# Kernel optimization log

Hardware: AMD Instinct MI355X
Metric: run time of the kernel (lower is better)

## Reference

```python
import jax, jax.numpy as jnp
import numpy as np

N_NODES = 40000
N_EDGES = 480000
MULT = 64
NUM_SPECIES = 5
N_BASIS = 8
MLP_HIDDEN = 64
AVG_NEIGH = 12.0

INV8 = float(1.0 / np.sqrt(8.0))
INV64 = float(1.0 / np.sqrt(64.0))
INV128 = float(1.0 / np.sqrt(128.0))


def _poly_envelope(x):
    # e3nn.poly_envelope(5, 2) == DimeNet-style cutoff with p=6:
    # f(0)=1, first 5 derivatives zero at 0, f and 2 derivatives zero at 1.
    u = 1.0 - 28.0 * x**6 + 48.0 * x**7 - 21.0 * x**8
    return jnp.where(x < 1.0, u, 0.0)


def setup_inputs() -> dict:
    key = jax.random.key(0)
    ks = jax.random.split(key, 15)
    vectors = jax.random.uniform(ks[0], (N_EDGES, 3), jnp.float32, -0.5, 0.5)
    node_scalars = jax.random.normal(ks[1], (N_NODES, MULT), jnp.float32)
    node_vectors = jax.random.normal(ks[2], (N_NODES, MULT, 3), jnp.float32)
    node_specie = jax.random.randint(ks[3], (N_NODES,), 0, NUM_SPECIES)
    senders = jax.random.randint(ks[4], (N_EDGES,), 0, N_NODES)
    receivers = jax.random.randint(ks[5], (N_EDGES,), 0, N_NODES)
    # learned params (e3nn Linear weights ~ N(0,1), fwd divides by sqrt(fan_in))
    W_up_s = jax.random.normal(ks[6], (MULT, MULT), jnp.float32)
    W_up_v = jax.random.normal(ks[7], (MULT, MULT), jnp.float32)
    W_skip_s = jax.random.normal(ks[8], (NUM_SPECIES, MULT, 2 * MULT), jnp.float32)
    W_skip_v = jax.random.normal(ks[9], (NUM_SPECIES, MULT, MULT), jnp.float32)
    W_mlp1 = jax.random.normal(ks[10], (N_BASIS, MLP_HIDDEN), jnp.float32)
    W_mlp2 = jax.random.normal(ks[11], (MLP_HIDDEN, MLP_HIDDEN), jnp.float32)
    W_mlp3 = jax.random.normal(ks[12], (MLP_HIDDEN, 4 * MULT), jnp.float32)
    W_down_s = jax.random.normal(ks[13], (2 * MULT, 2 * MULT), jnp.float32)
    W_down_v = jax.random.normal(ks[14], (2 * MULT, MULT), jnp.float32)
    return dict(vectors=vectors, node_scalars=node_scalars, node_vectors=node_vectors,
                node_specie=node_specie, senders=senders, receivers=receivers,
                W_up_s=W_up_s, W_up_v=W_up_v, W_skip_s=W_skip_s, W_skip_v=W_skip_v,
                W_mlp1=W_mlp1, W_mlp2=W_mlp2, W_mlp3=W_mlp3,
                W_down_s=W_down_s, W_down_v=W_down_v)


def reference(vectors, node_scalars, node_vectors, node_specie, senders, receivers,
              W_up_s, W_up_v, W_skip_s, W_skip_v, W_mlp1, W_mlp2, W_mlp3,
              W_down_s, W_down_v):
    N = node_scalars.shape[0]
    # self-connection: species-indexed linear ('skip_tp'), output 128x0e + 64x1o
    sc_s = jnp.einsum('ni,nio->no', node_scalars, W_skip_s[node_specie]) * INV64
    sc_v = jnp.einsum('nic,nio->noc', node_vectors, W_skip_v[node_specie]) * INV64
    # linear_up (irreps-wise linear, 64x0e+64x1o -> same)
    h_s = (node_scalars @ W_up_s) * INV64
    h_v = jnp.einsum('nic,io->noc', node_vectors, W_up_v) * INV64
    # gather by sender
    m_s = h_s[senders]                       # [E,64]
    m_v = h_v[senders]                       # [E,64,3]
    # spherical harmonics l=1, normalize=True, component norm: sqrt(3)*r_hat
    lengths = jnp.linalg.norm(vectors, axis=1, keepdims=True)   # [E,1]
    safe_len = jnp.where(lengths == 0.0, 1.0, lengths)
    Y = jnp.sqrt(3.0) * vectors / safe_len                      # [E,3]
    # sparse CG tensor product (component norm): 0e x 1o -> 1o, 1o x 1o -> 0e
    tp_1o = m_s[:, :, None] * Y[:, None, :]                     # [E,64,3]
    tp_0e = jnp.einsum('eic,ec->ei', m_v, Y) / jnp.sqrt(3.0)    # [E,64]
    # concatenate + regroup -> 128x0e + 128x1o
    msg_s = jnp.concatenate([m_s, tp_0e], axis=1)               # [E,128]
    msg_v = jnp.concatenate([m_v, tp_1o], axis=1)               # [E,128,3]
    # radial basis (bessel, x_max=1) * smooth envelope
    k = jnp.arange(1, N_BASIS + 1, dtype=jnp.float32)
    bes = jnp.sqrt(2.0) * jnp.sin(k * jnp.pi * safe_len) / safe_len  # [E,8]
    rb = jnp.where(lengths == 0.0, 0.0, bes * _poly_envelope(lengths))
    h = jax.nn.swish((rb @ W_mlp1) * INV8)
    h = jax.nn.swish((h @ W_mlp2) * INV64)
    mix = (h @ W_mlp3) * INV64                                  # [E,256]
    msg_s = msg_s * mix[:, :128]
    msg_v = msg_v * mix[:, 128:, None]
    # scatter-add to receivers, normalize by sqrt(avg_num_neighbors)
    inv_sqrt_nn = 1.0 / np.sqrt(AVG_NEIGH)
    agg_s = jax.ops.segment_sum(msg_s, receivers, num_segments=N) * inv_sqrt_nn
    agg_v = jax.ops.segment_sum(msg_v, receivers, num_segments=N) * inv_sqrt_nn
    # linear_down to 128x0e + 64x1o, plus self-connection
    d_s = (agg_s @ W_down_s) * INV128 + sc_s                    # [N,128]
    d_v = jnp.einsum('nic,io->noc', agg_v, W_down_v) * INV128 + sc_v  # [N,64,3]
    # gate: first 64 scalars kept (swish), last 64 gate the vectors (swish)
    out_s = jax.nn.swish(d_s[:, :MULT])
    gates = jax.nn.swish(d_s[:, MULT:])
    out_v = d_v * gates[:, :, None]
    return jnp.concatenate([out_s, out_v.reshape(N, MULT * 3)], axis=1)  # [N,256]
```

## Files before the change

kernel.cpp:

```cpp
#include <hip/hip_runtime.h>
#include <hip/hip_bf16.h>

#define N_NODES 40000
#define N_EDGES 480000
#define SEG 2
#define SEG_E (N_EDGES / SEG)
#define SEG_TILES (SEG_E / 16)
#define SCAN_BLOCKS 157
#define TPW 2

typedef short bf16x8 __attribute__((ext_vector_type(8)));
typedef float f32x4 __attribute__((ext_vector_type(4)));

__device__ __forceinline__ float bf2f(__hip_bfloat16 x) { return __bfloat162float(x); }

__device__ __forceinline__ float swishf(float x) { return x / (1.0f + __expf(-x)); }

__device__ __forceinline__ float bflo(unsigned u) { union { unsigned u; float f; } w; w.u = u << 16; return w.f; }
__device__ __forceinline__ float bfhi(unsigned u) { union { unsigned u; float f; } w; w.u = u & 0xffff0000u; return w.f; }
__device__ __forceinline__ float bfu(unsigned short u) { union { unsigned u; float f; } w; w.u = ((unsigned)u) << 16; return w.f; }

__device__ __forceinline__ unsigned short f2bf_bits(float x) {
    union { __hip_bfloat16 h; unsigned short u; } c; c.h = __float2bfloat16(x); return c.u;
}

__constant__ const float INV8 = 0.35355339059327373f;
__constant__ const float INV64 = 0.125f;
__constant__ const float INV128 = 0.08838834764831845f;
__constant__ const float INV_NN = 0.2886751345948129f;
__constant__ const float SQRT2 = 1.4142135623730951f;
__constant__ const float SQRT3 = 1.7320508075688772f;
__constant__ const float INV_SQRT3 = 0.5773502691896258f;
__constant__ const float PI_F = 3.14159265358979323846f;

__device__ __forceinline__ float LDf(const void* p, size_t i, bool f32) {
    float v;
    if (f32) v = ((const float*)p)[i];
    else     v = bf2f(((const __hip_bfloat16*)p)[i]);
    return v;
}
__device__ __forceinline__ void load_f8r(const void* p, size_t i, bool f32, float* out) {
    if (f32) {
        const float4* q4 = (const float4*)((const float*)p + i);
        float4 a = q4[0], b = q4[1];
        out[0] = a.x; out[1] = a.y; out[2] = a.z; out[3] = a.w;
        out[4] = b.x; out[5] = b.y; out[6] = b.z; out[7] = b.w;
    } else {
        bf16x8 v = *(const bf16x8*)((const unsigned short*)p + i);
        #pragma unroll
        for (int j = 0; j < 8; j++) out[j] = bfu((unsigned short)v[j]);
    }
}

__global__ void detect_kernel(const unsigned short* __restrict__ w, int* __restrict__ flag) {
    int lane = threadIdx.x;
    int cnt = 0;
    for (int i = lane; i < 2048; i += 64) {
        unsigned e = (w[2 * i] >> 7) & 0xFF;
        if (e >= 110 && e <= 133) cnt++;
    }
    #pragma unroll
    for (int off = 32; off > 0; off >>= 1) cnt += __shfl_down(cnt, off, 64);
    if (lane == 0) *flag = (cnt > 1024) ? 1 : 0;
}

__global__ __launch_bounds__(256) void wprep_kernel(
    const void* __restrict__ W_up_s, const void* __restrict__ W_up_v,
    const void* __restrict__ W_skip_s, const void* __restrict__ W_skip_v,
    const void* __restrict__ W_down_s, const void* __restrict__ W_down_v,
    const void* __restrict__ W_mlp2, const void* __restrict__ W_mlp3,
    unsigned short* __restrict__ Wup_sq, unsigned short* __restrict__ Wup_vq,
    unsigned short* __restrict__ Wq_s, unsigned short* __restrict__ Wq_v,
    unsigned short* __restrict__ W2q, unsigned short* __restrict__ W3q,
    const int* __restrict__ flag)
{
    bool f32 = (*flag == 0);
    const float SC = INV128 * INV_NN;
    int gid = blockIdx.x * 256 + threadIdx.x;
    int gs = gridDim.x * 256;
    for (int i = gid; i < 4096; i += gs) {
        int o = i & 63, k = i >> 6;
        Wup_sq[o * 72 + k] = f2bf_bits(LDf(W_up_s, k * 64 + o, f32) * INV64);
        Wup_vq[o * 72 + k] = f2bf_bits(LDf(W_up_v, k * 64 + o, f32) * INV64);
    }
    for (int i = gid; i < 5 * 128 * 192; i += gs) {
        int sp = i / 24576, r = i - sp * 24576;
        int o = r / 192, k = r - o * 192;
        float w = (k < 128) ? LDf(W_down_s, k * 128 + o, f32) * SC
                            : LDf(W_skip_s, sp * 8192 + (k - 128) * 128 + o, f32) * INV64;
        Wq_s[sp * 25600 + o * 200 + k] = f2bf_bits(w);
    }
    for (int i = gid; i < 5 * 64 * 192; i += gs) {
        int sp = i / 12288, r = i - sp * 12288;
        int o = r / 192, k = r - o * 192;
        float w = (k < 128) ? LDf(W_down_v, k * 64 + o, f32) * SC
                            : LDf(W_skip_v, sp * 4096 + (k - 128) * 64 + o, f32) * INV64;
        Wq_v[sp * 12800 + o * 200 + k] = f2bf_bits(w);
    }
    for (int i = gid; i < 16384; i += gs) {
        int o = i & 255, k = i >> 8;
        W3q[o * 72 + k] = f2bf_bits(LDf(W_mlp3, k * 256 + o, f32));
    }
    for (int i = gid; i < 4096; i += gs) {
        int o = i & 63, k = i >> 6;
        W2q[o * 72 + k] = f2bf_bits(LDf(W_mlp2, k * 64 + o, f32));
    }
}

__global__ __launch_bounds__(256) void hist_kernel(const int* __restrict__ receivers,
                                                   int* __restrict__ cnt) {
    int e = blockIdx.x * 256 + threadIdx.x;
    if (e < N_EDGES) atomicAdd(&cnt[receivers[e]], 1);
}

__global__ __launch_bounds__(256) void partial_kernel(const int* __restrict__ cnt,
                                                      int* __restrict__ partials) {
    __shared__ int red[4];
    int idx = blockIdx.x * 256 + threadIdx.x;
    int v = (idx < N_NODES) ? cnt[idx] : 0;
    #pragma unroll
    for (int off = 32; off > 0; off >>= 1) v += __shfl_down(v, off, 64);
    int wave = threadIdx.x >> 6, lane = threadIdx.x & 63;
    if (lane == 0) red[wave] = v;
    __syncthreads();
    if (threadIdx.x == 0) partials[blockIdx.x] = red[0] + red[1] + red[2] + red[3];
}

__global__ __launch_bounds__(256) void scanp_kernel(const int* __restrict__ partials,
                                                    int* __restrict__ pscan) {
    __shared__ int buf[256];
    int t = threadIdx.x;
    int v = (t < SCAN_BLOCKS) ? partials[t] : 0;
    buf[t] = v;
    __syncthreads();
    for (int off = 1; off < 256; off <<= 1) {
        int tmp = (t >= off) ? buf[t - off] : 0;
        __syncthreads();
        buf[t] += tmp;
        __syncthreads();
    }
    if (t < SCAN_BLOCKS) pscan[t] = buf[t] - v;
}

__global__ __launch_bounds__(256) void offs_kernel(const int* __restrict__ cnt,
                                                   const int* __restrict__ pscan,
                                                   int* __restrict__ offs,
                                                   int* __restrict__ cursor) {
    __shared__ int buf[256];
    int b = blockIdx.x, t = threadIdx.x;
    int idx = b * 256 + t;
    int v = (idx < N_NODES) ? cnt[idx] : 0;
    buf[t] = v;
    __syncthreads();
    for (int off = 1; off < 256; off <<= 1) {
        int tmp = (t >= off) ? buf[t - off] : 0;
        __syncthreads();
        buf[t] += tmp;
        __syncthreads();
    }
    int exc = buf[t] - v + pscan[b];
    if (idx < N_NODES) { offs[idx] = exc; cursor[idx] = exc; }
    if (idx == N_NODES - 1) offs[N_NODES] = exc + v;
}

__global__ __launch_bounds__(256) void scatter_kernel(const int* __restrict__ receivers,
                                                      const int* __restrict__ senders,
                                                      const void* __restrict__ vectors,
                                                      int* __restrict__ cursor,
                                                      int* __restrict__ sorted_snd,
                                                      float4* __restrict__ sorted_vec,
                                                      const int* __restrict__ flag) {
    bool f32 = (*flag == 0);
    int e = blockIdx.x * 256 + threadIdx.x;
    if (e < N_EDGES) {
        float vx = LDf(vectors, (size_t)e * 3 + 0, f32);
        float vy = LDf(vectors, (size_t)e * 3 + 1, f32);
        float vz = LDf(vectors, (size_t)e * 3 + 2, f32);
        int p = atomicAdd(&cursor[receivers[e]], 1);
        sorted_snd[p] = senders[e];
        sorted_vec[p] = float4{vx, vy, vz, 0.f};
    }
}

__global__ __launch_bounds__(256) void hist5_kernel(const int* __restrict__ specie,
                                                    int* __restrict__ cnt5) {
    int n = blockIdx.x * 256 + threadIdx.x;
    int lane = threadIdx.x & 63;
    int sp = (n < N_NODES) ? specie[n] : -1;
    #pragma unroll
    for (int s = 0; s < 5; s++) {
        unsigned long long mask = __ballot(sp == s);
        if (mask != 0ull) {
            int leader = __builtin_ctzll(mask);
            if (lane == leader) atomicAdd(&cnt5[s], __popcll(mask));
        }
    }
}

__global__ void scan5_kernel(const int* __restrict__ cnt5, int* __restrict__ sp_offs,
                             int* __restrict__ cursor5, int* __restrict__ tile_info) {
    if (threadIdx.x != 0 || blockIdx.x != 0) return;
    int run = 0, tb = 0;
    for (int s = 0; s < 5; s++) {
        sp_offs[s] = run; cursor5[s] = run;
        tile_info[s] = tb;
        int c = cnt5[s];
        int T = (c + 15) >> 4;
        tile_info[8 + s] = T;
        tb += (T + 3) >> 2;
        run += c;
    }
    sp_offs[5] = run;
    tile_info[5] = tb;
}

__global__ __launch_bounds__(256) void scatter5_kernel(const int* __restrict__ specie,
                                                       int* __restrict__ cursor5,
                                                       int* __restrict__ sorted_node) {
    int n = blockIdx.x * 256 + threadIdx.x;
    int lane = threadIdx.x & 63;
    int sp = (n < N_NODES) ? specie[n] : -1;
    #pragma unroll
    for (int s = 0; s < 5; s++) {
        unsigned long long mask = __ballot(sp == s);
        if (mask != 0ull) {
            int leader = __builtin_ctzll(mask);
            int base = 0;
            if (lane == leader) base = atomicAdd(&cursor5[s], __popcll(mask));
            base = __shfl(base, leader);
            if (sp == s) {
                int prefix = __popcll(mask & ((1ull << lane) - 1ull));
                sorted_node[base + prefix] = n;
            }
        }
    }
}

__global__ __launch_bounds__(256) void node_up_kernel(
    const void* __restrict__ node_scalars,
    const void* __restrict__ node_vectors,
    const unsigned short* __restrict__ Wup_sq,
    const unsigned short* __restrict__ Wup_vq,
    unsigned short* __restrict__ hbuf,
    unsigned short* __restrict__ ns_b,
    unsigned short* __restrict__ nv_t,
    const int* __restrict__ flag)
{
    bool f32 = (*flag == 0);
    __shared__ __align__(16) unsigned short WsT[64 * 72];
    __shared__ __align__(16) unsigned short WvT[64 * 72];
    int tid = threadIdx.x;
    for (int i = tid; i < 576; i += 256) {
        ((uint4*)WsT)[i] = ((const uint4*)Wup_sq)[i];
        ((uint4*)WvT)[i] = ((const uint4*)Wup_vq)[i];
    }
    __syncthreads();
    int wave = tid >> 6, lane = tid & 63;
    int m = lane & 15, q = lane >> 4;
    int base = (blockIdx.x * 4 + wave) * 16;

    f32x4 accS[4];
    f32x4 accV[3][4];
    #pragma unroll
    for (int t = 0; t < 4; t++) {
        accS[t] = f32x4{0.f, 0.f, 0.f, 0.f};
        #pragma unroll
        for (int c = 0; c < 3; c++) accV[c][t] = f32x4{0.f, 0.f, 0.f, 0.f};
    }

    #pragma unroll
    for (int kk = 0; kk < 2; kk++) {
        int i0 = kk * 32 + 8 * q;
        float fs[8];
        load_f8r(node_scalars, (size_t)(base + m) * 64 + i0, f32, fs);
        bf16x8 aS;
        #pragma unroll
        for (int j = 0; j < 8; j++) aS[j] = (short)f2bf_bits(fs[j]);
        *(bf16x8*)(ns_b + (size_t)(base + m) * 64 + i0) = aS;
        float fv[24];
        size_t vbase = (size_t)(base + m) * 192 + (size_t)i0 * 3;
        load_f8r(node_vectors, vbase,      f32, fv);
        load_f8r(node_vectors, vbase + 8,  f32, fv + 8);
        load_f8r(node_vectors, vbase + 16, f32, fv + 16);
        bf16x8 aV[3];
        #pragma unroll
        for (int c = 0; c < 3; c++) {
            #pragma unroll
            for (int j = 0; j < 8; j++) aV[c][j] = (short)f2bf_bits(fv[3 * j + c]);
            *(bf16x8*)(nv_t + (size_t)c * N_NODES * 64 + (size_t)(base + m) * 64 + i0) = aV[c];
        }
        #pragma unroll
        for (int t = 0; t < 4; t++) {
            bf16x8 bS = *(const bf16x8*)(WsT + (16 * t + m) * 72 + kk * 32 + 8 * q);
            bf16x8 bV = *(const bf16x8*)(WvT + (16 * t + m) * 72 + kk * 32 + 8 * q);
            accS[t]    = __builtin_amdgcn_mfma_f32_16x16x32_bf16(aS,    bS, accS[t],    0, 0, 0);
            accV[0][t] = __builtin_amdgcn_mfma_f32_16x16x32_bf16(aV[0], bV, accV[0][t], 0, 0, 0);
            accV[1][t] = __builtin_amdgcn_mfma_f32_16x16x32_bf16(aV[1], bV, accV[1][t], 0, 0, 0);
            accV[2][t] = __builtin_amdgcn_mfma_f32_16x16x32_bf16(aV[2], bV, accV[2][t], 0, 0, 0);
        }
    }
    #pragma unroll
    for (int t = 0; t < 4; t++) {
        #pragma unroll
        for (int r = 0; r < 4; r++) {
            uint2 pk;
            pk.x = (unsigned)f2bf_bits(accS[t][r])    | ((unsigned)f2bf_bits(accV[0][t][r]) << 16);
            pk.y = (unsigned)f2bf_bits(accV[1][t][r]) | ((unsigned)f2bf_bits(accV[2][t][r]) << 16);
            *(uint2*)(hbuf + (size_t)(base + 4 * q + r) * 256 + (16 * t + m) * 4) = pk;
        }
    }
}

__global__ __launch_bounds__(512) void mlp_kernel(
    const float4* __restrict__ sorted_vec,
    const void* __restrict__ W1,
    const unsigned short* __restrict__ W2q,
    const unsigned short* __restrict__ W3q,
    unsigned short* __restrict__ mixseg,
    unsigned short* __restrict__ yq,
    int p_lo,
    const int* __restrict__ flag)
{
    bool f32 = (*flag == 0);
    __shared__ __align__(16) unsigned short W3T[256 * 72];
    __shared__ __align__(16) unsigned short W2T[64 * 72];
    __shared__ unsigned short hbl[8 * 64 * 18];
    int tid = threadIdx.x;
    for (int i = tid; i < 2304; i += 512) ((uint4*)W3T)[i] = ((const uint4*)W3q)[i];
    for (int i = tid; i < 576; i += 512)  ((uint4*)W2T)[i] = ((const uint4*)W2q)[i];
    __syncthreads();
    int wave = tid >> 6, lane = tid & 63;
    int m = lane & 15, q = lane >> 4;
    unsigned short* hb = hbl + wave * (64 * 18);
    f32x4 zero4 = {0.f, 0.f, 0.f, 0.f};

    bf16x8 a1f[4];
    #pragma unroll
    for (int t = 0; t < 4; t++) {
        #pragma unroll
        for (int j = 0; j < 8; j++) a1f[t][j] = 0;
        if (q == 0) {
            #pragma unroll
            for (int j = 0; j < 8; j++)
                a1f[t][j] = (short)f2bf_bits(LDf(W1, j * 64 + 16 * t + m, f32));
        }
    }

    int tile0 = (blockIdx.x * 8 + wave) * TPW;
    #pragma unroll 1
    for (int tt = 0; tt < TPW; tt++) {
        int tile = tile0 + tt;
        if (tile >= SEG_TILES) break;
        int p = p_lo + tile * 16 + m;

        float4 sv = sorted_vec[p];
        float vx = sv.x, vy = sv.y, vz = sv.z;
        float len2 = vx * vx + vy * vy + vz * vz;
        float len = sqrtf(len2);
        float Yx = 0.f, Yy = 0.f, Yz = 0.f;
        float rb[8];
        if (len > 0.f) {
            float inv = 1.f / len;
            Yx = SQRT3 * vx * inv; Yy = SQRT3 * vy * inv; Yz = SQRT3 * vz * inv;
            float x6 = len2 * len2 * len2;
            float env = (len < 1.f) ? fmaf(x6, fmaf(len, fmaf(len, -21.f, 48.f), -28.f), 1.f) : 0.f;
            float c = SQRT2 * inv * env;
            #pragma unroll
            for (int k = 0; k < 8; k++) rb[k] = c * __sinf((float)(k + 1) * PI_F * len);
        } else {
            #pragma unroll
            for (int k = 0; k < 8; k++) rb[k] = 0.f;
        }
        if (q == 0) {
            uint2 yw;
            yw.x = f2bf_bits(Yx) | ((unsigned)f2bf_bits(Yy) << 16);
            yw.y = f2bf_bits(Yz);
            *(uint2*)(yq + (size_t)p * 4) = yw;
        }

        bf16x8 b_rb;
        #pragma unroll
        for (int j = 0; j < 8; j++) b_rb[j] = (q == 0) ? (short)f2bf_bits(rb[j]) : (short)0;
        #pragma unroll
        for (int t = 0; t < 4; t++) {
            f32x4 c = __builtin_amdgcn_mfma_f32_16x16x32_bf16(a1f[t], b_rb, zero4, 0, 0, 0);
            #pragma unroll
            for (int r = 0; r < 4; r++)
                hb[(16 * t + 4 * q + r) * 18 + m] = f2bf_bits(swishf(c[r] * INV8));
        }
        bf16x8 b2[2];
        #pragma unroll
        for (int h = 0; h < 2; h++)
            #pragma unroll
            for (int j = 0; j < 8; j++)
                b2[h][j] = (short)hb[(32 * h + 8 * q + j) * 18 + m];
        #pragma unroll
        for (int t = 0; t < 4; t++) {
            bf16x8 a0 = *(const bf16x8*)(W2T + (16 * t + m) * 72 + 8 * q);
            bf16x8 a1 = *(const bf16x8*)(W2T + (16 * t + m) * 72 + 32 + 8 * q);
            f32x4 c = __builtin_amdgcn_mfma_f32_16x16x32_bf16(a0, b2[0], zero4, 0, 0, 0);
            c = __builtin_amdgcn_mfma_f32_16x16x32_bf16(a1, b2[1], c, 0, 0, 0);
            #pragma unroll
            for (int r = 0; r < 4; r++)
                hb[(16 * t + 4 * q + r) * 18 + m] = f2bf_bits(swishf(c[r] * INV64));
        }
        bf16x8 b3[2];
        #pragma unroll
        for (int h = 0; h < 2; h++)
            #pragma unroll
            for (int j = 0; j < 8; j++)
                b3[h][j] = (short)hb[(32 * h + 8 * q + j) * 18 + m];
        size_t rowbase = ((size_t)(tile * 16 + m)) * 256;
        #pragma unroll
        for (int t3 = 0; t3 < 16; t3++) {
            bf16x8 a0 = *(const bf16x8*)(W3T + (16 * t3 + m) * 72 + 8 * q);
            bf16x8 a1 = *(const bf16x8*)(W3T + (16 * t3 + m) * 72 + 32 + 8 * q);
            f32x4 c = __builtin_amdgcn_mfma_f32_16x16x32_bf16(a0, b3[0], zero4, 0, 0, 0);
            c = __builtin_amdgcn_mfma_f32_16x16x32_bf16(a1, b3[1], c, 0, 0, 0);
            uint2 v;
            v.x = f2bf_bits(c[0] * INV64) | ((unsigned)f2bf_bits(c[1] * INV64) << 16);
            v.y = f2bf_bits(c[2] * INV64) | ((unsigned)f2bf_bits(c[3] * INV64) << 16);
            *(uint2*)(mixseg + rowbase + 16 * t3 + 4 * q) = v;
        }
    }
}

__global__ __launch_bounds__(256) void agg_kernel(
    const unsigned short* __restrict__ hbuf,
    const int* __restrict__ sorted_snd,
    const unsigned short* __restrict__ mixseg,
    const unsigned short* __restrict__ yq,
    const int* __restrict__ offs,
    unsigned short* __restrict__ agg_s_b,
    unsigned short* __restrict__ agg_v_b,
    int slo, int shi)
{
    int tid = threadIdx.x, wave = tid >> 6, lane = tid & 63;
    int n = blockIdx.x * 4 + wave;
    if (n >= N_NODES) return;
    int beg = __builtin_amdgcn_readfirstlane(offs[n]);
    int end = __builtin_amdgcn_readfirstlane(offs[n + 1]);
    int lo = beg > slo ? beg : slo;
    int hi = end < shi ? end : shi;
    bool owner = (beg >= slo && beg < shi) || (beg >= shi && shi == N_EDGES);
    if (!owner && hi <= lo) return;
    unsigned short* aS = agg_s_b + (size_t)n * 128;
    unsigned short* aV = agg_v_b + (size_t)n * 384;
    float s0, s1, v0, v1, v2, v3, v4, v5;
    if (owner) {
        s0 = s1 = v0 = v1 = v2 = v3 = v4 = v5 = 0.f;
    } else {
        s0 = bfu(aS[lane]); s1 = bfu(aS[64 + lane]);
        v0 = bfu(aV[lane]); v1 = bfu(aV[64 + lane]); v2 = bfu(aV[128 + lane]);
        v3 = bfu(aV[192 + lane]); v4 = bfu(aV[256 + lane]); v5 = bfu(aV[320 + lane]);
    }
    for (int chunk = lo; chunk < hi; chunk += 64) {
        int cc = hi - chunk; if (cc > 64) cc = 64;
        int sv = (lane < cc) ? sorted_snd[chunk + lane] : 0;
        int i = 0;
        for (; i + 3 < cc; i += 4) {
            uint2 h[4]; uint2 yw[4];
            float mx[4][4];
            #pragma unroll
            for (int u = 0; u < 4; u++) {
                int snd = __builtin_amdgcn_readlane(sv, i + u);
                int p = chunk + i + u;
                h[u] = *(const uint2*)(hbuf + (size_t)snd * 256 + lane * 4);
                const unsigned short* mp = mixseg + (size_t)(p - slo) * 256;
                mx[u][0] = bfu(mp[lane]);       mx[u][1] = bfu(mp[64 + lane]);
                mx[u][2] = bfu(mp[128 + lane]); mx[u][3] = bfu(mp[192 + lane]);
                yw[u] = *(const uint2*)(yq + (size_t)p * 4);
            }
            #pragma unroll
            for (int u = 0; u < 4; u++) {
                float m_s = bflo(h[u].x), mv0 = bfhi(h[u].x), mv1 = bflo(h[u].y), mv2 = bfhi(h[u].y);
                float Yx = bflo(yw[u].x), Yy = bfhi(yw[u].x), Yz = bflo(yw[u].y);
                float tp0 = (mv0 * Yx + mv1 * Yy + mv2 * Yz) * INV_SQRT3;
                s0 = fmaf(m_s, mx[u][0], s0);
                s1 = fmaf(tp0, mx[u][1], s1);
                float t1 = m_s * mx[u][3];
                v0 = fmaf(mv0, mx[u][2], v0); v1 = fmaf(t1, Yx, v1);
                v2 = fmaf(mv1, mx[u][2], v2); v3 = fmaf(t1, Yy, v3);
                v4 = fmaf(mv2, mx[u][2], v4); v5 = fmaf(t1, Yz, v5);
            }
        }
        for (; i < cc; i++) {
            int snd = __builtin_amdgcn_readlane(sv, i);
            int p = chunk + i;
            uint2 hbv = *(const uint2*)(hbuf + (size_t)snd * 256 + lane * 4);
            const unsigned short* mp = mixseg + (size_t)(p - slo) * 256;
            float mix0 = bfu(mp[lane]), mix1 = bfu(mp[64 + lane]);
            float mix2 = bfu(mp[128 + lane]), mix3 = bfu(mp[192 + lane]);
            uint2 yw = *(const uint2*)(yq + (size_t)p * 4);
            float m_s = bflo(hbv.x), mv0 = bfhi(hbv.x), mv1 = bflo(hbv.y), mv2 = bfhi(hbv.y);
            float Yx = bflo(yw.x), Yy = bfhi(yw.x), Yz = bflo(yw.y);
            float tp0 = (mv0 * Yx + mv1 * Yy + mv2 * Yz) * INV_SQRT3;
            s0 = fmaf(m_s, mix0, s0);
            s1 = fmaf(tp0, mix1, s1);
            float t1 = m_s * mix3;
            v0 = fmaf(mv0, mix2, v0); v1 = fmaf(t1, Yx, v1);
            v2 = fmaf(mv1, mix2, v2); v3 = fmaf(t1, Yy, v3);
            v4 = fmaf(mv2, mix2, v4); v5 = fmaf(t1, Yz, v5);
        }
    }
    aS[lane] = f2bf_bits(s0); aS[64 + lane] = f2bf_bits(s1);
    aV[lane] = f2bf_bits(v0); aV[64 + lane] = f2bf_bits(v1); aV[128 + lane] = f2bf_bits(v2);
    aV[192 + lane] = f2bf_bits(v3); aV[256 + lane] = f2bf_bits(v4); aV[320 + lane] = f2bf_bits(v5);
}

__global__ __launch_bounds__(256) void node_final_kernel(
    const unsigned short* __restrict__ Wq_s,
    const unsigned short* __restrict__ Wq_v,
    const unsigned short* __restrict__ ns_b,
    const unsigned short* __restrict__ nv_t,
    const unsigned short* __restrict__ agg_s_b,
    const unsigned short* __restrict__ agg_v_b,
    const int* __restrict__ sorted_node,
    const int* __restrict__ sp_offs,
    const int* __restrict__ tile_info,
    void* __restrict__ out,
    const int* __restrict__ flag)
{
    bool f32 = (*flag == 0);
    int b = blockIdx.x;
    if (b >= tile_info[5]) return;
    __shared__ __align__(16) unsigned short As[128 * 200];
    __shared__ __align__(16) unsigned short Av[64 * 200];
    int sp = 0;
    #pragma unroll
    for (int s = 1; s < 5; s++) if (b >= tile_info[s]) sp = s;
    int tid = threadIdx.x;
    const uint4* ps = (const uint4*)(Wq_s + (size_t)sp * 25600);
    for (int i = tid; i < 3200; i += 256) ((uint4*)As)[i] = ps[i];
    const uint4* pv = (const uint4*)(Wq_v + (size_t)sp * 12800);
    for (int i = tid; i < 1600; i += 256) ((uint4*)Av)[i] = pv[i];
    __syncthreads();
    int wave = tid >> 6, lane = tid & 63;
    int m = lane & 15, q = lane >> 4;
    int T = tile_info[8 + sp];
    int tl = (b - tile_info[sp]) * 4 + wave;
    if (tl >= T) return;
    int row = sp_offs[sp] + tl * 16;
    int cnt = sp_offs[sp + 1] - row; if (cnt > 16) cnt = 16;
    int mm = (m < cnt) ? m : 0;
    int node = sorted_node[row + mm];

    bf16x8 bs[6];
    {
        const unsigned short* a = agg_s_b + (size_t)node * 128;
        #pragma unroll
        for (int f = 0; f < 4; f++) bs[f] = *(const bf16x8*)(a + f * 32 + q * 8);
        const unsigned short* s = ns_b + (size_t)node * 64;
        #pragma unroll
        for (int f = 0; f < 2; f++) bs[4 + f] = *(const bf16x8*)(s + f * 32 + q * 8);
    }
    bf16x8 bv[3][6];
    #pragma unroll
    for (int c = 0; c < 3; c++) {
        const unsigned short* a = agg_v_b + (size_t)node * 384 + c * 128;
        #pragma unroll
        for (int f = 0; f < 4; f++) bv[c][f] = *(const bf16x8*)(a + f * 32 + q * 8);
        const unsigned short* s = nv_t + (size_t)c * N_NODES * 64 + (size_t)node * 64;
        #pragma unroll
        for (int f = 0; f < 2; f++) bv[c][4 + f] = *(const bf16x8*)(s + f * 32 + q * 8);
    }
    f32x4 z4 = {0.f, 0.f, 0.f, 0.f};
    float gate[4][4];
    #pragma unroll
    for (int t = 0; t < 4; t++) {
        f32x4 c = z4;
        #pragma unroll
        for (int f = 0; f < 6; f++) {
            bf16x8 a = *(const bf16x8*)(As + (16 * (4 + t) + m) * 200 + f * 32 + q * 8);
            c = __builtin_amdgcn_mfma_f32_16x16x32_bf16(a, bs[f], c, 0, 0, 0);
        }
        #pragma unroll
        for (int r = 0; r < 4; r++) gate[t][r] = swishf(c[r]);
    }
    #pragma unroll
    for (int t = 0; t < 4; t++) {
        f32x4 c = z4;
        #pragma unroll
        for (int f = 0; f < 6; f++) {
            bf16x8 a = *(const bf16x8*)(As + (16 * t + m) * 200 + f * 32 + q * 8);
            c = __builtin_amdgcn_mfma_f32_16x16x32_bf16(a, bs[f], c, 0, 0, 0);
        }
        if (m < cnt) {
            size_t base = (size_t)node * 256 + 16 * t + 4 * q;
            if (f32) {
                float4 o4 = { swishf(c[0]), swishf(c[1]), swishf(c[2]), swishf(c[3]) };
                *(float4*)((float*)out + base) = o4;
            } else {
                uint2 o2;
                o2.x = f2bf_bits(swishf(c[0])) | ((unsigned)f2bf_bits(swishf(c[1])) << 16);
                o2.y = f2bf_bits(swishf(c[2])) | ((unsigned)f2bf_bits(swishf(c[3])) << 16);
                *(uint2*)((unsigned short*)out + base) = o2;
            }
        }
    }
    #pragma unroll
    for (int t = 0; t < 4; t++) {
        f32x4 c0 = z4, c1 = z4, c2 = z4;
        #pragma unroll
        for (int f = 0; f < 6; f++) {
            bf16x8 a = *(const bf16x8*)(Av + (16 * t + m) * 200 + f * 32 + q * 8);
            c0 = __builtin_amdgcn_mfma_f32_16x16x32_bf16(a, bv[0][f], c0, 0, 0, 0);
            c1 = __builtin_amdgcn_mfma_f32_16x16x32_bf16(a, bv[1][f], c1, 0, 0, 0);
            c2 = __builtin_amdgcn_mfma_f32_16x16x32_bf16(a, bv[2][f], c2, 0, 0, 0);
        }
        if (m < cnt) {
            #pragma unroll
            for (int r = 0; r < 4; r++) {
                float g = gate[t][r];
                int o = 16 * t + 4 * q + r;
                size_t base = (size_t)node * 256 + 64 + (size_t)o * 3;
                if (f32) {
                    ((float*)out)[base + 0] = c0[r] * g;
                    ((float*)out)[base + 1] = c1[r] * g;
                    ((float*)out)[base + 2] = c2[r] * g;
                } else {
                    ((__hip_bfloat16*)out)[base + 0] = __float2bfloat16(c0[r] * g);
                    ((__hip_bfloat16*)out)[base + 1] = __float2bfloat16(c1[r] * g);
                    ((__hip_bfloat16*)out)[base + 2] = __float2bfloat16(c2[r] * g);
                }
            }
        }
    }
}

extern "C" void kernel_launch(void* const* d_in, const int* in_sizes, int n_in,
                              void* d_out, int out_size, void* d_ws, size_t ws_size,
                              hipStream_t stream) {
    const void* vectors      = d_in[0];
    const void* node_scalars = d_in[1];
    const void* node_vectors = d_in[2];
    const int* node_specie   = (const int*)d_in[3];
    const int* senders       = (const int*)d_in[4];
    const int* receivers     = (const int*)d_in[5];
    const void* W_up_s       = d_in[6];
    const void* W_up_v       = d_in[7];
    const void* W_skip_s     = d_in[8];
    const void* W_skip_v     = d_in[9];
    const void* W_mlp1       = d_in[10];
    const void* W_mlp2       = d_in[11];
    const void* W_mlp3       = d_in[12];
    const void* W_down_s     = d_in[13];
    const void* W_down_v     = d_in[14];

    char* ws = (char*)d_ws;
    size_t off = 0;
    auto alloc = [&](size_t bytes) { void* p = ws + off; off += (bytes + 255) & ~(size_t)255; return p; };
    unsigned short* hbuf     = (unsigned short*)alloc((size_t)N_NODES * 256 * 2);
    unsigned short* ns_b     = (unsigned short*)alloc((size_t)N_NODES * 64 * 2);
    unsigned short* nv_t     = (unsigned short*)alloc((size_t)N_NODES * 192 * 2);
    unsigned short* agg_s_b  = (unsigned short*)alloc((size_t)N_NODES * 128 * 2);
    unsigned short* agg_v_b  = (unsigned short*)alloc((size_t)N_NODES * 384 * 2);
    unsigned short* mixseg   = (unsigned short*)alloc((size_t)SEG_E * 256 * 2);
    unsigned short* yq       = (unsigned short*)alloc((size_t)N_EDGES * 4 * 2);
    float4* sorted_vec       = (float4*)alloc((size_t)N_EDGES * 16);
    unsigned short* Wup_sq   = (unsigned short*)alloc((size_t)64 * 72 * 2);
    unsigned short* Wup_vq   = (unsigned short*)alloc((size_t)64 * 72 * 2);
    unsigned short* Wq_s     = (unsigned short*)alloc((size_t)5 * 128 * 200 * 2);
    unsigned short* Wq_v     = (unsigned short*)alloc((size_t)5 * 64 * 200 * 2);
    unsigned short* W2q      = (unsigned short*)alloc((size_t)64 * 72 * 2);
    unsigned short* W3q      = (unsigned short*)alloc((size_t)256 * 72 * 2);
    int* cnt        = (int*)alloc((size_t)(N_NODES + 8) * 4);
    int* cnt5       = cnt + N_NODES;
    int* offs       = (int*)alloc((size_t)(N_NODES + 1) * 4);
    int* cursor     = (int*)alloc((size_t)N_NODES * 4);
    int* sorted_snd = (int*)alloc((size_t)N_EDGES * 4);
    int* sorted_node= (int*)alloc((size_t)N_NODES * 4);
    int* sp_offs    = (int*)alloc(16 * 4);
    int* cursor5    = (int*)alloc(16 * 4);
    int* tile_info  = (int*)alloc(16 * 4);
    int* partials   = (int*)alloc((size_t)(SCAN_BLOCKS + 1) * 4);
    int* pscan      = (int*)alloc((size_t)(SCAN_BLOCKS + 1) * 4);
    int* flag       = (int*)alloc(4);

    detect_kernel<<<dim3(1), dim3(64), 0, stream>>>((const unsigned short*)W_up_s, flag);
    hipMemsetAsync(cnt, 0, (size_t)(N_NODES + 8) * 4, stream);

    wprep_kernel<<<dim3(64), dim3(256), 0, stream>>>(
        W_up_s, W_up_v, W_skip_s, W_skip_v, W_down_s, W_down_v, W_mlp2, W_mlp3,
        Wup_sq, Wup_vq, Wq_s, Wq_v, W2q, W3q, flag);

    hist_kernel<<<dim3(1875), dim3(256), 0, stream>>>(receivers, cnt);
    partial_kernel<<<dim3(SCAN_BLOCKS), dim3(256), 0, stream>>>(cnt, partials);
    scanp_kernel<<<dim3(1), dim3(256), 0, stream>>>(partials, pscan);
    offs_kernel<<<dim3(SCAN_BLOCKS), dim3(256), 0, stream>>>(cnt, pscan, offs, cursor);
    scatter_kernel<<<dim3(1875), dim3(256), 0, stream>>>(receivers, senders, vectors,
                                                         cursor, sorted_snd, sorted_vec, flag);

    hist5_kernel<<<dim3(157), dim3(256), 0, stream>>>(node_specie, cnt5);
    scan5_kernel<<<dim3(1), dim3(64), 0, stream>>>(cnt5, sp_offs, cursor5, tile_info);
    scatter5_kernel<<<dim3(157), dim3(256), 0, stream>>>(node_specie, cursor5, sorted_node);

    node_up_kernel<<<dim3(625), dim3(256), 0, stream>>>(
        node_scalars, node_vectors, Wup_sq, Wup_vq, hbuf, ns_b, nv_t, flag);

    const int MLP_BLOCKS = (SEG_TILES + 8 * TPW - 1) / (8 * TPW);
    for (int s = 0; s < SEG; s++) {
        int p_lo = s * SEG_E;
        mlp_kernel<<<dim3(MLP_BLOCKS), dim3(512), 0, stream>>>(
            sorted_vec, W_mlp1, W2q, W3q, mixseg, yq, p_lo, flag);
        agg_kernel<<<dim3(10000), dim3(256), 0, stream>>>(
            hbuf, sorted_snd, mixseg, yq, offs, agg_s_b, agg_v_b, p_lo, p_lo + SEG_E);
    }

    node_final_kernel<<<dim3(640), dim3(256), 0, stream>>>(
        Wq_s, Wq_v, ns_b, nv_t, agg_s_b, agg_v_b,
        sorted_node, sp_offs, tile_info, d_out, flag);
}
```

Measured before the change: 506.8 us.

## Precompute radial basis in scatter and interleave mix layout for vectorized loads

Moves the edge-length, spherical-harmonic and Bessel/envelope computation into the scatter kernel, which now writes packed bf16 Y and radial-basis arrays in sorted order, so the MLP kernel only loads 8 bf16 values per edge. The MLP output is re-laid out so each lane's four mix values sit next to each other, letting the aggregation kernel fetch them with one 8-byte load instead of four scattered 2-byte loads. Tiles per wave rise from 2 to 4. The trade-off is extra transcendental work in the scatter kernel and a changed intermediate format.

```diff
diff --git a/kernel.cpp b/kernel.cpp
--- a/kernel.cpp
+++ b/kernel.cpp
@@ -7,7 +7,7 @@
 #define SEG_E (N_EDGES / SEG)
 #define SEG_TILES (SEG_E / 16)
 #define SCAN_BLOCKS 157
-#define TPW 2
+#define TPW 4
 
 typedef short bf16x8 __attribute__((ext_vector_type(8)));
 typedef float f32x4 __attribute__((ext_vector_type(4)));
@@ -168,7 +168,8 @@
                                                       const void* __restrict__ vectors,
                                                       int* __restrict__ cursor,
                                                       int* __restrict__ sorted_snd,
-                                                      float4* __restrict__ sorted_vec,
+                                                      unsigned short* __restrict__ yq,
+                                                      unsigned short* __restrict__ rbq,
                                                       const int* __restrict__ flag) {
     bool f32 = (*flag == 0);
     int e = blockIdx.x * 256 + threadIdx.x;
@@ -176,9 +177,32 @@
         float vx = LDf(vectors, (size_t)e * 3 + 0, f32);
         float vy = LDf(vectors, (size_t)e * 3 + 1, f32);
         float vz = LDf(vectors, (size_t)e * 3 + 2, f32);
+        float len2 = vx * vx + vy * vy + vz * vz;
+        float len = sqrtf(len2);
+        float Yx = 0.f, Yy = 0.f, Yz = 0.f;
+        float rb[8];
+        if (len > 0.f) {
+            float inv = 1.f / len;
+            Yx = SQRT3 * vx * inv; Yy = SQRT3 * vy * inv; Yz = SQRT3 * vz * inv;
+            float x6 = len2 * len2 * len2;
+            float env = (len < 1.f) ? fmaf(x6, fmaf(len, fmaf(len, -21.f, 48.f), -28.f), 1.f) : 0.f;
+            float c = SQRT2 * inv * env;
+            #pragma unroll
+            for (int k = 0; k < 8; k++) rb[k] = c * __sinf((float)(k + 1) * PI_F * len);
+        } else {
+            #pragma unroll
+            for (int k = 0; k < 8; k++) rb[k] = 0.f;
+        }
         int p = atomicAdd(&cursor[receivers[e]], 1);
         sorted_snd[p] = senders[e];
-        sorted_vec[p] = float4{vx, vy, vz, 0.f};
+        uint2 yw;
+        yw.x = f2bf_bits(Yx) | ((unsigned)f2bf_bits(Yy) << 16);
+        yw.y = f2bf_bits(Yz);
+        *(uint2*)(yq + (size_t)p * 4) = yw;
+        bf16x8 r8;
+        #pragma unroll
+        for (int k = 0; k < 8; k++) r8[k] = (short)f2bf_bits(rb[k]);
+        *(bf16x8*)(rbq + (size_t)p * 8) = r8;
     }
 }
 
@@ -312,12 +336,11 @@
 }
 
 __global__ __launch_bounds__(512) void mlp_kernel(
-    const float4* __restrict__ sorted_vec,
+    const unsigned short* __restrict__ rbq,
     const void* __restrict__ W1,
     const unsigned short* __restrict__ W2q,
     const unsigned short* __restrict__ W3q,
-    unsigned short* __restrict__ mixseg,
-    unsigned short* __restrict__ yq,
+    unsigned short* __restrict__ mixp,
     int p_lo,
     const int* __restrict__ flag)
 {
@@ -353,34 +376,11 @@
         if (tile >= SEG_TILES) break;
         int p = p_lo + tile * 16 + m;
 
-        float4 sv = sorted_vec[p];
-        float vx = sv.x, vy = sv.y, vz = sv.z;
-        float len2 = vx * vx + vy * vy + vz * vz;
-        float len = sqrtf(len2);
-        float Yx = 0.f, Yy = 0.f, Yz = 0.f;
-        float rb[8];
-        if (len > 0.f) {
-            float inv = 1.f / len;
-            Yx = SQRT3 * vx * inv; Yy = SQRT3 * vy * inv; Yz = SQRT3 * vz * inv;
-            float x6 = len2 * len2 * len2;
-            float env = (len < 1.f) ? fmaf(x6, fmaf(len, fmaf(len, -21.f, 48.f), -28.f), 1.f) : 0.f;
-            float c = SQRT2 * inv * env;
-            #pragma unroll
-            for (int k = 0; k < 8; k++) rb[k] = c * __sinf((float)(k + 1) * PI_F * len);
-        } else {
-            #pragma unroll
-            for (int k = 0; k < 8; k++) rb[k] = 0.f;
-        }
-        if (q == 0) {
-            uint2 yw;
-            yw.x = f2bf_bits(Yx) | ((unsigned)f2bf_bits(Yy) << 16);
-            yw.y = f2bf_bits(Yz);
-            *(uint2*)(yq + (size_t)p * 4) = yw;
-        }
-
         bf16x8 b_rb;
         #pragma unroll
-        for (int j = 0; j < 8; j++) b_rb[j] = (q == 0) ? (short)f2bf_bits(rb[j]) : (short)0;
+        for (int j = 0; j < 8; j++) b_rb[j] = 0;
+        if (q == 0) b_rb = *(const bf16x8*)(rbq + (size_t)p * 8);
+
         #pragma unroll
         for (int t = 0; t < 4; t++) {
             f32x4 c = __builtin_amdgcn_mfma_f32_16x16x32_bf16(a1f[t], b_rb, zero4, 0, 0, 0);
@@ -410,17 +410,27 @@
             #pragma unroll
             for (int j = 0; j < 8; j++)
                 b3[h][j] = (short)hb[(32 * h + 8 * q + j) * 18 + m];
-        size_t rowbase = ((size_t)(tile * 16 + m)) * 256;
-        #pragma unroll
-        for (int t3 = 0; t3 < 16; t3++) {
-            bf16x8 a0 = *(const bf16x8*)(W3T + (16 * t3 + m) * 72 + 8 * q);
-            bf16x8 a1 = *(const bf16x8*)(W3T + (16 * t3 + m) * 72 + 32 + 8 * q);
-            f32x4 c = __builtin_amdgcn_mfma_f32_16x16x32_bf16(a0, b3[0], zero4, 0, 0, 0);
-            c = __builtin_amdgcn_mfma_f32_16x16x32_bf16(a1, b3[1], c, 0, 0, 0);
-            uint2 v;
-            v.x = f2bf_bits(c[0] * INV64) | ((unsigned)f2bf_bits(c[1] * INV64) << 16);
-            v.y = f2bf_bits(c[2] * INV64) | ((unsigned)f2bf_bits(c[3] * INV64) << 16);
-            *(uint2*)(mixseg + rowbase + 16 * t3 + 4 * q) = v;
+        size_t ebase = ((size_t)(tile * 16 + m)) * 256;
+        #pragma unroll
+        for (int t3p = 0; t3p < 4; t3p++) {
+            f32x4 cg[4];
+            #pragma unroll
+            for (int g = 0; g < 4; g++) {
+                int t3 = t3p + 4 * g;
+                bf16x8 a0 = *(const bf16x8*)(W3T + (16 * t3 + m) * 72 + 8 * q);
+                bf16x8 a1 = *(const bf16x8*)(W3T + (16 * t3 + m) * 72 + 32 + 8 * q);
+                f32x4 c = __builtin_amdgcn_mfma_f32_16x16x32_bf16(a0, b3[0], zero4, 0, 0, 0);
+                cg[g] = __builtin_amdgcn_mfma_f32_16x16x32_bf16(a1, b3[1], c, 0, 0, 0);
+            }
+            #pragma unroll
+            for (int r = 0; r < 4; r += 2) {
+                uint4 w;
+                w.x = f2bf_bits(cg[0][r] * INV64)     | ((unsigned)f2bf_bits(cg[1][r] * INV64) << 16);
+                w.y = f2bf_bits(cg[2][r] * INV64)     | ((unsigned)f2bf_bits(cg[3][r] * INV64) << 16);
+                w.z = f2bf_bits(cg[0][r + 1] * INV64) | ((unsigned)f2bf_bits(cg[1][r + 1] * INV64) << 16);
+                w.w = f2bf_bits(cg[2][r + 1] * INV64) | ((unsigned)f2bf_bits(cg[3][r + 1] * INV64) << 16);
+                *(uint4*)(mixp + ebase + (size_t)(16 * t3p + 4 * q + r) * 4) = w;
+            }
         }
     }
 }
@@ -428,7 +438,7 @@
 __global__ __launch_bounds__(256) void agg_kernel(
     const unsigned short* __restrict__ hbuf,
     const int* __restrict__ sorted_snd,
-    const unsigned short* __restrict__ mixseg,
+    const unsigned short* __restrict__ mixp,
     const unsigned short* __restrict__ yq,
     const int* __restrict__ offs,
     unsigned short* __restrict__ agg_s_b,
@@ -459,40 +469,39 @@
         int sv = (lane < cc) ? sorted_snd[chunk + lane] : 0;
         int i = 0;
         for (; i + 3 < cc; i += 4) {
-            uint2 h[4]; uint2 yw[4];
-            float mx[4][4];
+            uint2 h[4], mxw[4], yw[4];
             #pragma unroll
             for (int u = 0; u < 4; u++) {
                 int snd = __builtin_amdgcn_readlane(sv, i + u);
                 int p = chunk + i + u;
-                h[u] = *(const uint2*)(hbuf + (size_t)snd * 256 + lane * 4);
-                const unsigned short* mp = mixseg + (size_t)(p - slo) * 256;
-                mx[u][0] = bfu(mp[lane]);       mx[u][1] = bfu(mp[64 + lane]);
-                mx[u][2] = bfu(mp[128 + lane]); mx[u][3] = bfu(mp[192 + lane]);
-                yw[u] = *(const uint2*)(yq + (size_t)p * 4);
+                h[u]   = *(const uint2*)(hbuf + (size_t)snd * 256 + lane * 4);
+                mxw[u] = *(const uint2*)(mixp + (size_t)(p - slo) * 256 + lane * 4);
+                yw[u]  = *(const uint2*)(yq + (size_t)p * 4);
             }
             #pragma unroll
             for (int u = 0; u < 4; u++) {
                 float m_s = bflo(h[u].x), mv0 = bfhi(h[u].x), mv1 = bflo(h[u].y), mv2 = bfhi(h[u].y);
+                float mix0 = bflo(mxw[u].x), mix1 = bfhi(mxw[u].x);
+                float mix2 = bflo(mxw[u].y), mix3 = bfhi(mxw[u].y);
                 float Yx = bflo(yw[u].x), Yy = bfhi(yw[u].x), Yz = bflo(yw[u].y);
                 float tp0 = (mv0 * Yx + mv1 * Yy + mv2 * Yz) * INV_SQRT3;
-                s0 = fmaf(m_s, mx[u][0], s0);
-                s1 = fmaf(tp0, mx[u][1], s1);
-                float t1 = m_s * mx[u][3];
-                v0 = fmaf(mv0, mx[u][2], v0); v1 = fmaf(t1, Yx, v1);
-                v2 = fmaf(mv1, mx[u][2], v2); v3 = fmaf(t1, Yy, v3);
-                v4 = fmaf(mv2, mx[u][2], v4); v5 = fmaf(t1, Yz, v5);
+                s0 = fmaf(m_s, mix0, s0);
+                s1 = fmaf(tp0, mix1, s1);
+                float t1 = m_s * mix3;
+                v0 = fmaf(mv0, mix2, v0); v1 = fmaf(t1, Yx, v1);
+                v2 = fmaf(mv1, mix2, v2); v3 = fmaf(t1, Yy, v3);
+                v4 = fmaf(mv2, mix2, v4); v5 = fmaf(t1, Yz, v5);
             }
         }
         for (; i < cc; i++) {
             int snd = __builtin_amdgcn_readlane(sv, i);
             int p = chunk + i;
             uint2 hbv = *(const uint2*)(hbuf + (size_t)snd * 256 + lane * 4);
-            const unsigned short* mp = mixseg + (size_t)(p - slo) * 256;
-            float mix0 = bfu(mp[lane]), mix1 = bfu(mp[64 + lane]);
-            float mix2 = bfu(mp[128 + lane]), mix3 = bfu(mp[192 + lane]);
-            uint2 yw = *(const uint2*)(yq + (size_t)p * 4);
+            uint2 mxw = *(const uint2*)(mixp + (size_t)(p - slo) * 256 + lane * 4);
+            uint2 yw  = *(const uint2*)(yq + (size_t)p * 4);
             float m_s = bflo(hbv.x), mv0 = bfhi(hbv.x), mv1 = bflo(hbv.y), mv2 = bfhi(hbv.y);
+            float mix0 = bflo(mxw.x), mix1 = bfhi(mxw.x);
+            float mix2 = bflo(mxw.y), mix3 = bfhi(mxw.y);
             float Yx = bflo(yw.x), Yy = bfhi(yw.x), Yz = bflo(yw.y);
             float tp0 = (mv0 * Yx + mv1 * Yy + mv2 * Yz) * INV_SQRT3;
             s0 = fmaf(m_s, mix0, s0);
@@ -655,9 +664,9 @@
     unsigned short* nv_t     = (unsigned short*)alloc((size_t)N_NODES * 192 * 2);
     unsigned short* agg_s_b  = (unsigned short*)alloc((size_t)N_NODES * 128 * 2);
     unsigned short* agg_v_b  = (unsigned short*)alloc((size_t)N_NODES * 384 * 2);
-    unsigned short* mixseg   = (unsigned short*)alloc((size_t)SEG_E * 256 * 2);
+    unsigned short* mixp     = (unsigned short*)alloc((size_t)SEG_E * 256 * 2);
     unsigned short* yq       = (unsigned short*)alloc((size_t)N_EDGES * 4 * 2);
-    float4* sorted_vec       = (float4*)alloc((size_t)N_EDGES * 16);
+    unsigned short* rbq      = (unsigned short*)alloc((size_t)N_EDGES * 8 * 2);
     unsigned short* Wup_sq   = (unsigned short*)alloc((size_t)64 * 72 * 2);
     unsigned short* Wup_vq   = (unsigned short*)alloc((size_t)64 * 72 * 2);
     unsigned short* Wq_s     = (unsigned short*)alloc((size_t)5 * 128 * 200 * 2);
@@ -678,7 +687,7 @@
     int* flag       = (int*)alloc(4);
 
     detect_kernel<<<dim3(1), dim3(64), 0, stream>>>((const unsigned short*)W_up_s, flag);
-    hipMemsetAsync(cnt, 0, (size_t)(N_NODES + 8) * 4, stream);
+    (void)hipMemsetAsync(cnt, 0, (size_t)(N_NODES + 8) * 4, stream);
 
     wprep_kernel<<<dim3(64), dim3(256), 0, stream>>>(
         W_up_s, W_up_v, W_skip_s, W_skip_v, W_down_s, W_down_v, W_mlp2, W_mlp3,
@@ -689,7 +698,7 @@
     scanp_kernel<<<dim3(1), dim3(256), 0, stream>>>(partials, pscan);
     offs_kernel<<<dim3(SCAN_BLOCKS), dim3(256), 0, stream>>>(cnt, pscan, offs, cursor);
     scatter_kernel<<<dim3(1875), dim3(256), 0, stream>>>(receivers, senders, vectors,
-                                                         cursor, sorted_snd, sorted_vec, flag);
+                                                         cursor, sorted_snd, yq, rbq, flag);
 
     hist5_kernel<<<dim3(157), dim3(256), 0, stream>>>(node_specie, cnt5);
     scan5_kernel<<<dim3(1), dim3(64), 0, stream>>>(cnt5, sp_offs, cursor5, tile_info);
@@ -702,9 +711,9 @@
     for (int s = 0; s < SEG; s++) {
         int p_lo = s * SEG_E;
         mlp_kernel<<<dim3(MLP_BLOCKS), dim3(512), 0, stream>>>(
-            sorted_vec, W_mlp1, W2q, W3q, mixseg, yq, p_lo, flag);
+            rbq, W_mlp1, W2q, W3q, mixp, p_lo, flag);
         agg_kernel<<<dim3(10000), dim3(256), 0, stream>>>(
-            hbuf, sorted_snd, mixseg, yq, offs, agg_s_b, agg_v_b, p_lo, p_lo + SEG_E);
+            hbuf, sorted_snd, mixp, yq, offs, agg_s_b, agg_v_b, p_lo, p_lo + SEG_E);
     }
 
     node_final_kernel<<<dim3(640), dim3(256), 0, stream>>>(
```

Measured after the change: 489.3 us. -3.5%, faster.
